# Optimization experiments

Measured on AMD Instinct MI355X. Metric: run time of the kernel, lower is better.

Reference implementation:

```python
import jax, jax.numpy as jnp
import numpy as np

N_NODES = 100000
N_EDGES = 600000
DIM = 128


def mish(v):
    return v * jnp.tanh(jax.nn.softplus(v))


def setup_inputs() -> dict:
    key = jax.random.key(0)
    ks = jax.random.split(key, 10)
    x = jax.random.normal(ks[0], (N_NODES, DIM), dtype=jnp.float32)
    edge_attr = jax.random.normal(ks[1], (N_EDGES, DIM), dtype=jnp.float32)
    # build edges with src < dst guaranteed (so the torch mask edge_index[0]<edge_index[1] is all True)
    a = jax.random.randint(ks[2], (N_EDGES,), 0, N_NODES - 1)
    b = jax.random.randint(ks[3], (N_EDGES,), 0, N_NODES - 1)
    src = jnp.minimum(a, b)
    dst = jnp.maximum(a, b) + (src == jnp.maximum(a, b)).astype(a.dtype)  # fix ties, stays < N_NODES
    edge_index = jnp.stack([src, dst]).astype(jnp.int64)
    s1 = 1.0 / np.sqrt(2 * DIM)
    s2 = 1.0 / np.sqrt(DIM)
    eW1 = jax.random.uniform(ks[4], (2 * DIM, DIM), jnp.float32, -s1, s1)
    eW2 = jax.random.uniform(ks[5], (DIM, DIM), jnp.float32, -s2, s2)
    nW1 = jax.random.uniform(ks[6], (2 * DIM, DIM), jnp.float32, -s1, s1)
    nW2 = jax.random.uniform(ks[7], (DIM, DIM), jnp.float32, -s2, s2)
    zb = jnp.zeros((DIM,), jnp.float32)
    return {"x": x, "edge_attr": edge_attr, "edge_index": edge_index,
            "eW1": eW1, "eb1": zb, "eW2": eW2, "eb2": zb,
            "nW1": nW1, "nb1": zb, "nW2": nW2, "nb2": zb}


def reference(x, edge_attr, edge_index, eW1, eb1, eW2, eb2, nW1, nb1, nW2, nb2):
    src, dst = edge_index[0], edge_index[1]
    # mask src < dst is all-True by construction of edge_index (see setup_inputs)
    e_in = jnp.concatenate([edge_attr, x[src] + x[dst]], axis=-1)      # [E, 2d]
    e = mish(e_in @ eW1 + eb1) @ eW2 + eb2                             # [E, d]
    agg = jax.ops.segment_sum(edge_attr, dst, num_segments=N_NODES)    # scatter_sum over dst, padded to N
    x_in = jnp.concatenate([x, agg], axis=-1)                          # [N, 2d]
    x_out = mish(x_in @ nW1 + nb1) @ nW2 + nb2                         # [N, d]
    return x_out, e
```

## Files before the change

kernel.cpp:

```cpp
#include <hip/hip_runtime.h>

#define N_NODES 100000
#define N_EDGES 600000
#define DIM 128

typedef __attribute__((ext_vector_type(8))) short short8;
typedef __attribute__((ext_vector_type(4))) float floatx4;
typedef unsigned short ushort_t;

#define MFMA(a,b,c) __builtin_amdgcn_mfma_f32_16x16x32_bf16((a),(b),(c),0,0,0)

__device__ __forceinline__ void bar_sync() {
    asm volatile("s_waitcnt lgkmcnt(0)" ::: "memory");
    __builtin_amdgcn_s_barrier();
    asm volatile("" ::: "memory");
}

__device__ __forceinline__ unsigned short f2bf(float f) {
    unsigned int u = __float_as_uint(f);
    u += 0x7fffu + ((u >> 16) & 1u);
    return (unsigned short)(u >> 16);
}

__device__ __forceinline__ short8 pack8(const float4& a, const float4& b) {
    short8 r;
    r[0] = (short)f2bf(a.x); r[1] = (short)f2bf(a.y);
    r[2] = (short)f2bf(a.z); r[3] = (short)f2bf(a.w);
    r[4] = (short)f2bf(b.x); r[5] = (short)f2bf(b.y);
    r[6] = (short)f2bf(b.z); r[7] = (short)f2bf(b.w);
    return r;
}

__device__ __forceinline__ short8 addpack_bf(short8 a, short8 b) {
    short8 r;
    #pragma unroll
    for (int i = 0; i < 8; ++i) {
        const float fa = __uint_as_float(((unsigned int)(unsigned short)a[i]) << 16);
        const float fb = __uint_as_float(((unsigned int)(unsigned short)b[i]) << 16);
        r[i] = (short)f2bf(fa + fb);
    }
    return r;
}

__device__ __forceinline__ float mish_f(float v) {
    if (v > 30.0f) return v;
    float t = __expf(v);
    float z = 1.0f + t;
    float z2 = z * z;
    return v * (z2 - 1.0f) / (z2 + 1.0f);
}

__device__ __forceinline__ short8 load_bfrag(const float* __restrict__ W,
                                             int ct, int kt, int lane) {
    const float* p = W + (size_t)(kt * 32 + (lane >> 4) * 8) * DIM + ct * 16 + (lane & 15);
    short8 r;
    #pragma unroll
    for (int j = 0; j < 8; ++j) r[j] = (short)f2bf(p[(size_t)j * DIM]);
    return r;
}

__device__ __forceinline__ void mlp_core(
    const ushort_t* __restrict__ s_in, ushort_t* __restrict__ s_h,
    const short8 (&w1f)[8], const short8 (&w2f)[4],
    float b1v, float b2v, float* __restrict__ out, int wave, int lane)
{
    const int r0 = lane & 15, q = lane >> 4, sw = lane & 7;

    floatx4 acc0 = {0.f,0.f,0.f,0.f}, acc1 = acc0;
    #pragma unroll
    for (int kt = 0; kt < 8; ++kt) {
        const int g = kt * 4 + q;
        short8 a0 = *(const short8*)&s_in[r0 * 256 + (g ^ sw) * 8];
        short8 a1 = *(const short8*)&s_in[(16 + r0) * 256 + (g ^ sw) * 8];
        acc0 = MFMA(a0, w1f[kt], acc0);
        acc1 = MFMA(a1, w1f[kt], acc1);
    }

    const int colg = wave * 2 + (r0 >> 3);
    const int bq   = r0 & 7;
    #pragma unroll
    for (int i = 0; i < 4; ++i) {
        int row = q * 4 + i;
        s_h[row * 128 + (colg ^ (row & 7)) * 8 + bq] = f2bf(mish_f(acc0[i] + b1v));
        row += 16;
        s_h[row * 128 + (colg ^ (row & 7)) * 8 + bq] = f2bf(mish_f(acc1[i] + b1v));
    }
    bar_sync();

    floatx4 c0 = {0.f,0.f,0.f,0.f}, c1 = c0;
    #pragma unroll
    for (int kt = 0; kt < 4; ++kt) {
        const int g = kt * 4 + q;
        short8 a0 = *(const short8*)&s_h[r0 * 128 + (g ^ sw) * 8];
        short8 a1 = *(const short8*)&s_h[(16 + r0) * 128 + (g ^ sw) * 8];
        c0 = MFMA(a0, w2f[kt], c0);
        c1 = MFMA(a1, w2f[kt], c1);
    }

    const int col = wave * 16 + r0;
    #pragma unroll
    for (int i = 0; i < 4; ++i) {
        __builtin_nontemporal_store(c0[i] + b2v, &out[(size_t)(q * 4 + i) * DIM + col]);
        __builtin_nontemporal_store(c1[i] + b2v, &out[(size_t)(16 + q * 4 + i) * DIM + col]);
    }
}


__global__ __launch_bounds__(256)
void zero_u4(uint4* __restrict__ p, int n4) {
    const int i = blockIdx.x * 256 + threadIdx.x;
    if (i < n4) p[i] = make_uint4(0u, 0u, 0u, 0u);
}

__global__ __launch_bounds__(256)
void xbf_kernel(const float* __restrict__ x, ushort_t* __restrict__ x_bf) {
    const int i = blockIdx.x * 256 + threadIdx.x;
    const float* p = x + (size_t)i * 8;
    *(short8*)&x_bf[(size_t)i * 8] = pack8(*(const float4*)p, *(const float4*)(p + 4));
}

__global__ __launch_bounds__(256)
void hist_kernel(const int* __restrict__ dst_idx, int* __restrict__ deg) {
    const int e = blockIdx.x * 256 + threadIdx.x;
    if (e < N_EDGES) atomicAdd(&deg[dst_idx[e]], 1);
}

__global__ __launch_bounds__(1024)
void scan_a(const int* __restrict__ deg, int* __restrict__ tmp, int* __restrict__ partials) {
    __shared__ int sm[1024];
    const int t = threadIdx.x;
    const int i = blockIdx.x * 1024 + t;
    const int v = (i < N_NODES) ? deg[i] : 0;
    sm[t] = v; __syncthreads();
    for (int d = 1; d < 1024; d <<= 1) {
        int u = (t >= d) ? sm[t - d] : 0; __syncthreads();
        sm[t] += u; __syncthreads();
    }
    if (i < N_NODES) tmp[i] = sm[t] - v;
    if (t == 1023) partials[blockIdx.x] = sm[t];
}

__global__ __launch_bounds__(128)
void scan_b(const int* __restrict__ partials, int* __restrict__ poffs) {
    __shared__ int sm[128];
    const int t = threadIdx.x;
    const int v = (t < 98) ? partials[t] : 0;
    sm[t] = v; __syncthreads();
    for (int d = 1; d < 128; d <<= 1) {
        int u = (t >= d) ? sm[t - d] : 0; __syncthreads();
        sm[t] += u; __syncthreads();
    }
    poffs[t] = sm[t] - v;
}

__global__ __launch_bounds__(1024)
void scan_c(const int* __restrict__ tmp, const int* __restrict__ poffs,
            int* __restrict__ rowptr, int* __restrict__ cursor) {
    const int t = threadIdx.x;
    const int i = blockIdx.x * 1024 + t;
    if (i < N_NODES) {
        const int v = tmp[i] + poffs[blockIdx.x];
        rowptr[i] = v; cursor[i] = v;
    }
    if (i == 0) rowptr[N_NODES] = N_EDGES;
}

__global__ __launch_bounds__(256)
void scatter_kernel(const int* __restrict__ dst_idx, int* __restrict__ cursor,
                    int* __restrict__ perm) {
    const int e = blockIdx.x * 256 + threadIdx.x;
    if (e < N_EDGES) {
        const int pos = atomicAdd(&cursor[dst_idx[e]], 1);
        perm[pos] = e;
    }
}


__global__ __launch_bounds__(256)
void agg_kernel(const float* __restrict__ edge_attr, const int* __restrict__ rowptr,
                const int* __restrict__ perm, ushort_t* __restrict__ agg_bf) {
    const int g  = (blockIdx.x << 4) + (threadIdx.x >> 4);
    const int ln = threadIdx.x & 15;
    const int k0 = rowptr[g], k1 = rowptr[g + 1];
    float4 A0 = {0.f,0.f,0.f,0.f}, A1 = A0, B0 = A0, B1 = A0;
    int e0 = 0, e1 = 0, e2 = 0, e3 = 0;
    if (k0 < k1)     e0 = perm[k0];
    if (k0 + 1 < k1) e1 = perm[k0 + 1];
    if (k0 + 2 < k1) e2 = perm[k0 + 2];
    if (k0 + 3 < k1) e3 = perm[k0 + 3];
    int k = k0;
    for (; k + 3 < k1; k += 4) {
        const float* p0 = edge_attr + (size_t)e0 * DIM + ln * 8;
        const float* p1 = edge_attr + (size_t)e1 * DIM + ln * 8;
        const float* p2 = edge_attr + (size_t)e2 * DIM + ln * 8;
        const float* p3 = edge_attr + (size_t)e3 * DIM + ln * 8;
        const float4 a0 = *(const float4*)p0, a1 = *(const float4*)(p0 + 4);
        const float4 b0 = *(const float4*)p1, b1 = *(const float4*)(p1 + 4);
        const float4 c0 = *(const float4*)p2, c1 = *(const float4*)(p2 + 4);
        const float4 d0 = *(const float4*)p3, d1 = *(const float4*)(p3 + 4);
        if (k + 4 < k1) e0 = perm[k + 4];
        if (k + 5 < k1) e1 = perm[k + 5];
        if (k + 6 < k1) e2 = perm[k + 6];
        if (k + 7 < k1) e3 = perm[k + 7];
        A0.x += a0.x + c0.x; A0.y += a0.y + c0.y; A0.z += a0.z + c0.z; A0.w += a0.w + c0.w;
        A1.x += a1.x + c1.x; A1.y += a1.y + c1.y; A1.z += a1.z + c1.z; A1.w += a1.w + c1.w;
        B0.x += b0.x + d0.x; B0.y += b0.y + d0.y; B0.z += b0.z + d0.z; B0.w += b0.w + d0.w;
        B1.x += b1.x + d1.x; B1.y += b1.y + d1.y; B1.z += b1.z + d1.z; B1.w += b1.w + d1.w;
    }
    const int rem = k1 - k;
    if (rem > 0) {
        const float* p = edge_attr + (size_t)e0 * DIM + ln * 8;
        const float4 v0 = *(const float4*)p, v1 = *(const float4*)(p + 4);
        A0.x += v0.x; A0.y += v0.y; A0.z += v0.z; A0.w += v0.w;
        A1.x += v1.x; A1.y += v1.y; A1.z += v1.z; A1.w += v1.w;
    }
    if (rem > 1) {
        const float* p = edge_attr + (size_t)e1 * DIM + ln * 8;
        const float4 v0 = *(const float4*)p, v1 = *(const float4*)(p + 4);
        B0.x += v0.x; B0.y += v0.y; B0.z += v0.z; B0.w += v0.w;
        B1.x += v1.x; B1.y += v1.y; B1.z += v1.z; B1.w += v1.w;
    }
    if (rem > 2) {
        const float* p = edge_attr + (size_t)e2 * DIM + ln * 8;
        const float4 v0 = *(const float4*)p, v1 = *(const float4*)(p + 4);
        A0.x += v0.x; A0.y += v0.y; A0.z += v0.z; A0.w += v0.w;
        A1.x += v1.x; A1.y += v1.y; A1.z += v1.z; A1.w += v1.w;
    }
    A0.x += B0.x; A0.y += B0.y; A0.z += B0.z; A0.w += B0.w;
    A1.x += B1.x; A1.y += B1.y; A1.z += B1.z; A1.w += B1.w;
    *(short8*)&agg_bf[(size_t)g * DIM + ln * 8] = pack8(A0, A1);
}


__global__ __launch_bounds__(512)
void edge_kernel(const ushort_t* __restrict__ x_bf, const float* __restrict__ edge_attr,
                 const int* __restrict__ src_idx, const int* __restrict__ dst_idx,
                 const float* __restrict__ W1, const float* __restrict__ b1,
                 const float* __restrict__ W2, const float* __restrict__ b2,
                 float* __restrict__ e_out)
{
    __shared__ ushort_t s_in[32 * 256];
    __shared__ ushort_t s_h[32 * 128];
    const int tid = threadIdx.x, wave = tid >> 6, lane = tid & 63;

    short8 w1f[8], w2f[4];
    const float b1v = b1[wave * 16 + (lane & 15)];
    const float b2v = b2[wave * 16 + (lane & 15)];
    #pragma unroll
    for (int kt = 0; kt < 8; ++kt) w1f[kt] = load_bfrag(W1, wave, kt, lane);
    #pragma unroll
    for (int kt = 0; kt < 4; ++kt) w2f[kt] = load_bfrag(W2, wave, kt, lane);

    const int r = tid >> 4, gq = tid & 15, swr = r & 7;
    ushort_t* w_ea = &s_in[r * 256 + (gq ^ swr) * 8];
    ushort_t* w_x  = &s_in[r * 256 + ((16 + gq) ^ swr) * 8];

    const int ntiles = N_EDGES / 32;
    int t = blockIdx.x;
    float4 ea0, ea1;
    short8 xsb, xdb;
    if (t < ntiles) {
        const int k = t * 32 + r;
        const int s = src_idx[k], d = dst_idx[k];
        const float* pe = edge_attr + (size_t)k * DIM + gq * 8;
        ea0 = *(const float4*)pe; ea1 = *(const float4*)(pe + 4);
        xsb = *(const short8*)&x_bf[(size_t)s * DIM + gq * 8];
        xdb = *(const short8*)&x_bf[(size_t)d * DIM + gq * 8];
    }
    for (; t < ntiles; t += gridDim.x) {
        *(short8*)w_ea = pack8(ea0, ea1);
        *(short8*)w_x  = addpack_bf(xsb, xdb);

        const int tn = t + gridDim.x;
        const bool more = tn < ntiles;
        int sN = 0, dN = 0;
        if (more) {
            const float* pe = edge_attr + (size_t)(tn * 32 + r) * DIM + gq * 8;
            ea0 = *(const float4*)pe; ea1 = *(const float4*)(pe + 4);
            const int k = tn * 32 + r;
            sN = src_idx[k]; dN = dst_idx[k];
        }
        bar_sync();
        if (more) {
            xsb = *(const short8*)&x_bf[(size_t)sN * DIM + gq * 8];
            xdb = *(const short8*)&x_bf[(size_t)dN * DIM + gq * 8];
        }
        mlp_core(s_in, s_h, w1f, w2f, b1v, b2v,
                 e_out + (size_t)t * 32 * DIM, wave, lane);
    }
}

__global__ __launch_bounds__(512)
void node_kernel(const float* __restrict__ x, const ushort_t* __restrict__ agg_bf,
                 const float* __restrict__ W1, const float* __restrict__ b1,
                 const float* __restrict__ W2, const float* __restrict__ b2,
                 float* __restrict__ x_out)
{
    __shared__ ushort_t s_in[32 * 256];
    __shared__ ushort_t s_h[32 * 128];
    const int tid = threadIdx.x, wave = tid >> 6, lane = tid & 63;

    short8 w1f[8], w2f[4];
    const float b1v = b1[wave * 16 + (lane & 15)];
    const float b2v = b2[wave * 16 + (lane & 15)];
    #pragma unroll
    for (int kt = 0; kt < 8; ++kt) w1f[kt] = load_bfrag(W1, wave, kt, lane);
    #pragma unroll
    for (int kt = 0; kt < 4; ++kt) w2f[kt] = load_bfrag(W2, wave, kt, lane);

    const int r = tid >> 4, gq = tid & 15, swr = r & 7;
    ushort_t* w_xp = &s_in[r * 256 + (gq ^ swr) * 8];
    ushort_t* w_ag = &s_in[r * 256 + ((16 + gq) ^ swr) * 8];

    const int ntiles = N_NODES / 32;
    int t = blockIdx.x;
    float4 xv0, xv1;
    short8 ag;
    if (t < ntiles) {
        const float* px = x + (size_t)(t * 32 + r) * DIM + gq * 8;
        xv0 = *(const float4*)px; xv1 = *(const float4*)(px + 4);
        ag  = *(const short8*)&agg_bf[(size_t)(t * 32 + r) * DIM + gq * 8];
    }
    for (; t < ntiles; t += gridDim.x) {
        *(short8*)w_xp = pack8(xv0, xv1);
        *(short8*)w_ag = ag;
        const int tn = t + gridDim.x;
        if (tn < ntiles) {
            const float* px = x + (size_t)(tn * 32 + r) * DIM + gq * 8;
            xv0 = *(const float4*)px; xv1 = *(const float4*)(px + 4);
            ag  = *(const short8*)&agg_bf[(size_t)(tn * 32 + r) * DIM + gq * 8];
        }
        bar_sync();
        mlp_core(s_in, s_h, w1f, w2f, b1v, b2v,
                 x_out + (size_t)t * 32 * DIM, wave, lane);
    }
}

extern "C" void kernel_launch(void* const* d_in, const int* in_sizes, int n_in,
                              void* d_out, int out_size, void* d_ws, size_t ws_size,
                              hipStream_t stream)
{
    const float* x         = (const float*)d_in[0];
    const float* edge_attr = (const float*)d_in[1];
    const int*   ei        = (const int*)d_in[2];
    const float* eW1 = (const float*)d_in[3];
    const float* eb1 = (const float*)d_in[4];
    const float* eW2 = (const float*)d_in[5];
    const float* eb2 = (const float*)d_in[6];
    const float* nW1 = (const float*)d_in[7];
    const float* nb1 = (const float*)d_in[8];
    const float* nW2 = (const float*)d_in[9];
    const float* nb2 = (const float*)d_in[10];

    float* out   = (float*)d_out;
    float* x_out = out;
    float* e_out = out + (size_t)N_NODES * DIM;

    const int* src_idx = ei;
    const int* dst_idx = ei + N_EDGES;

    int* wsi      = (int*)d_ws;
    int* deg      = wsi;
    int* tmp      = wsi + 100352;
    int* rowptr   = wsi + 200704;
    int* cursor   = wsi + 301056;
    int* perm     = wsi + 401408;
    int* partials = wsi + 1001408;
    int* poffs    = wsi + 1001536;
    ushort_t* agg_bf = (ushort_t*)(wsi + 1001664);

    ushort_t* x_bf = (ushort_t*)x_out;

    const int egrid = (N_EDGES + 255) / 256;
    zero_u4       <<<dim3(98),    dim3(256),  0, stream>>>((uint4*)deg, 25088);
    xbf_kernel    <<<dim3(6250),  dim3(256),  0, stream>>>(x, x_bf);
    hist_kernel   <<<dim3(egrid), dim3(256),  0, stream>>>(dst_idx, deg);
    scan_a        <<<dim3(98),    dim3(1024), 0, stream>>>(deg, tmp, partials);
    scan_b        <<<dim3(1),     dim3(128),  0, stream>>>(partials, poffs);
    scan_c        <<<dim3(98),    dim3(1024), 0, stream>>>(tmp, poffs, rowptr, cursor);
    scatter_kernel<<<dim3(egrid), dim3(256),  0, stream>>>(dst_idx, cursor, perm);

    agg_kernel<<<dim3(6250), dim3(256), 0, stream>>>(edge_attr, rowptr, perm, agg_bf);

    edge_kernel<<<dim3(2048), dim3(512), 0, stream>>>(
        x_bf, edge_attr, src_idx, dst_idx, eW1, eb1, eW2, eb2, e_out);

    node_kernel<<<dim3(2048), dim3(512), 0, stream>>>(
        x, agg_bf, nW1, nb1, nW2, nb2, x_out);
}
```

Measured before the change: 363.2 us.

## Co-launch aggregation with edge MLP in one kernel, merge zero and bf16 cast

Puts the memory-bound segment-sum aggregation and the MFMA-bound edge MLP into one launch, with block-index ranges choosing the role, so the two can overlap on the GPU. It also merges the degree-zeroing and the x-to-bf16 conversion into a single launch. The goal is fewer launches and better overlap of bandwidth-bound and compute-bound work. In exchange, agg blocks now carry the edge kernel's 512-thread launch and LDS footprint, which can lower occupancy, and finish times across the two roles may be unbalanced.

```diff
diff --git a/kernel.cpp b/kernel.cpp
--- a/kernel.cpp
+++ b/kernel.cpp
@@ -3,6 +3,9 @@
 #define N_NODES 100000
 #define N_EDGES 600000
 #define DIM 128
+
+#define AGG_BLOCKS  1024
+#define EDGE_BLOCKS 2048
 
 typedef __attribute__((ext_vector_type(8))) short short8;
 typedef __attribute__((ext_vector_type(4))) float floatx4;
@@ -107,14 +110,15 @@
 
 
 __global__ __launch_bounds__(256)
-void zero_u4(uint4* __restrict__ p, int n4) {
-    const int i = blockIdx.x * 256 + threadIdx.x;
-    if (i < n4) p[i] = make_uint4(0u, 0u, 0u, 0u);
-}
-
-__global__ __launch_bounds__(256)
-void xbf_kernel(const float* __restrict__ x, ushort_t* __restrict__ x_bf) {
-    const int i = blockIdx.x * 256 + threadIdx.x;
+void zero_xbf_kernel(uint4* __restrict__ deg4, int n4,
+                     const float* __restrict__ x, ushort_t* __restrict__ x_bf) {
+    const int b = blockIdx.x;
+    if (b < 98) {
+        const int i = b * 256 + threadIdx.x;
+        if (i < n4) deg4[i] = make_uint4(0u, 0u, 0u, 0u);
+        return;
+    }
+    const int i = (b - 98) * 256 + threadIdx.x;
     const float* p = x + (size_t)i * 8;
     *(short8*)&x_bf[(size_t)i * 8] = pack8(*(const float4*)p, *(const float4*)(p + 4));
 }
@@ -176,72 +180,77 @@
 }
 
 
-__global__ __launch_bounds__(256)
-void agg_kernel(const float* __restrict__ edge_attr, const int* __restrict__ rowptr,
-                const int* __restrict__ perm, ushort_t* __restrict__ agg_bf) {
-    const int g  = (blockIdx.x << 4) + (threadIdx.x >> 4);
-    const int ln = threadIdx.x & 15;
-    const int k0 = rowptr[g], k1 = rowptr[g + 1];
-    float4 A0 = {0.f,0.f,0.f,0.f}, A1 = A0, B0 = A0, B1 = A0;
-    int e0 = 0, e1 = 0, e2 = 0, e3 = 0;
-    if (k0 < k1)     e0 = perm[k0];
-    if (k0 + 1 < k1) e1 = perm[k0 + 1];
-    if (k0 + 2 < k1) e2 = perm[k0 + 2];
-    if (k0 + 3 < k1) e3 = perm[k0 + 3];
-    int k = k0;
-    for (; k + 3 < k1; k += 4) {
-        const float* p0 = edge_attr + (size_t)e0 * DIM + ln * 8;
-        const float* p1 = edge_attr + (size_t)e1 * DIM + ln * 8;
-        const float* p2 = edge_attr + (size_t)e2 * DIM + ln * 8;
-        const float* p3 = edge_attr + (size_t)e3 * DIM + ln * 8;
-        const float4 a0 = *(const float4*)p0, a1 = *(const float4*)(p0 + 4);
-        const float4 b0 = *(const float4*)p1, b1 = *(const float4*)(p1 + 4);
-        const float4 c0 = *(const float4*)p2, c1 = *(const float4*)(p2 + 4);
-        const float4 d0 = *(const float4*)p3, d1 = *(const float4*)(p3 + 4);
-        if (k + 4 < k1) e0 = perm[k + 4];
-        if (k + 5 < k1) e1 = perm[k + 5];
-        if (k + 6 < k1) e2 = perm[k + 6];
-        if (k + 7 < k1) e3 = perm[k + 7];
-        A0.x += a0.x + c0.x; A0.y += a0.y + c0.y; A0.z += a0.z + c0.z; A0.w += a0.w + c0.w;
-        A1.x += a1.x + c1.x; A1.y += a1.y + c1.y; A1.z += a1.z + c1.z; A1.w += a1.w + c1.w;
-        B0.x += b0.x + d0.x; B0.y += b0.y + d0.y; B0.z += b0.z + d0.z; B0.w += b0.w + d0.w;
-        B1.x += b1.x + d1.x; B1.y += b1.y + d1.y; B1.z += b1.z + d1.z; B1.w += b1.w + d1.w;
-    }
-    const int rem = k1 - k;
-    if (rem > 0) {
-        const float* p = edge_attr + (size_t)e0 * DIM + ln * 8;
-        const float4 v0 = *(const float4*)p, v1 = *(const float4*)(p + 4);
-        A0.x += v0.x; A0.y += v0.y; A0.z += v0.z; A0.w += v0.w;
-        A1.x += v1.x; A1.y += v1.y; A1.z += v1.z; A1.w += v1.w;
-    }
-    if (rem > 1) {
-        const float* p = edge_attr + (size_t)e1 * DIM + ln * 8;
-        const float4 v0 = *(const float4*)p, v1 = *(const float4*)(p + 4);
-        B0.x += v0.x; B0.y += v0.y; B0.z += v0.z; B0.w += v0.w;
-        B1.x += v1.x; B1.y += v1.y; B1.z += v1.z; B1.w += v1.w;
-    }
-    if (rem > 2) {
-        const float* p = edge_attr + (size_t)e2 * DIM + ln * 8;
-        const float4 v0 = *(const float4*)p, v1 = *(const float4*)(p + 4);
-        A0.x += v0.x; A0.y += v0.y; A0.z += v0.z; A0.w += v0.w;
-        A1.x += v1.x; A1.y += v1.y; A1.z += v1.z; A1.w += v1.w;
-    }
-    A0.x += B0.x; A0.y += B0.y; A0.z += B0.z; A0.w += B0.w;
-    A1.x += B1.x; A1.y += B1.y; A1.z += B1.z; A1.w += B1.w;
-    *(short8*)&agg_bf[(size_t)g * DIM + ln * 8] = pack8(A0, A1);
-}
-
-
 __global__ __launch_bounds__(512)
-void edge_kernel(const ushort_t* __restrict__ x_bf, const float* __restrict__ edge_attr,
-                 const int* __restrict__ src_idx, const int* __restrict__ dst_idx,
-                 const float* __restrict__ W1, const float* __restrict__ b1,
-                 const float* __restrict__ W2, const float* __restrict__ b2,
-                 float* __restrict__ e_out)
+void edge_agg_kernel(const ushort_t* __restrict__ x_bf,
+                     const float* __restrict__ edge_attr,
+                     const int* __restrict__ src_idx, const int* __restrict__ dst_idx,
+                     const int* __restrict__ rowptr, const int* __restrict__ perm,
+                     const float* __restrict__ W1, const float* __restrict__ b1,
+                     const float* __restrict__ W2, const float* __restrict__ b2,
+                     float* __restrict__ e_out, ushort_t* __restrict__ agg_bf)
 {
     __shared__ ushort_t s_in[32 * 256];
     __shared__ ushort_t s_h[32 * 128];
-    const int tid = threadIdx.x, wave = tid >> 6, lane = tid & 63;
+    const int tid = threadIdx.x;
+
+    if (blockIdx.x < AGG_BLOCKS) {
+        const int sub = tid >> 4;
+        const int ln  = tid & 15;
+        for (int grp = blockIdx.x; grp < N_NODES / 32; grp += AGG_BLOCKS) {
+            const int g = grp * 32 + sub;
+            const int k0 = rowptr[g], k1 = rowptr[g + 1];
+            float4 A0 = {0.f,0.f,0.f,0.f}, A1 = A0, B0 = A0, B1 = A0;
+            int e0 = 0, e1 = 0, e2 = 0, e3 = 0;
+            if (k0 < k1)     e0 = perm[k0];
+            if (k0 + 1 < k1) e1 = perm[k0 + 1];
+            if (k0 + 2 < k1) e2 = perm[k0 + 2];
+            if (k0 + 3 < k1) e3 = perm[k0 + 3];
+            int k = k0;
+            for (; k + 3 < k1; k += 4) {
+                const float* p0 = edge_attr + (size_t)e0 * DIM + ln * 8;
+                const float* p1 = edge_attr + (size_t)e1 * DIM + ln * 8;
+                const float* p2 = edge_attr + (size_t)e2 * DIM + ln * 8;
+                const float* p3 = edge_attr + (size_t)e3 * DIM + ln * 8;
+                const float4 a0 = *(const float4*)p0, a1 = *(const float4*)(p0 + 4);
+                const float4 b0 = *(const float4*)p1, b1 = *(const float4*)(p1 + 4);
+                const float4 c0 = *(const float4*)p2, c1 = *(const float4*)(p2 + 4);
+                const float4 d0 = *(const float4*)p3, d1 = *(const float4*)(p3 + 4);
+                if (k + 4 < k1) e0 = perm[k + 4];
+                if (k + 5 < k1) e1 = perm[k + 5];
+                if (k + 6 < k1) e2 = perm[k + 6];
+                if (k + 7 < k1) e3 = perm[k + 7];
+                A0.x += a0.x + c0.x; A0.y += a0.y + c0.y; A0.z += a0.z + c0.z; A0.w += a0.w + c0.w;
+                A1.x += a1.x + c1.x; A1.y += a1.y + c1.y; A1.z += a1.z + c1.z; A1.w += a1.w + c1.w;
+                B0.x += b0.x + d0.x; B0.y += b0.y + d0.y; B0.z += b0.z + d0.z; B0.w += b0.w + d0.w;
+                B1.x += b1.x + d1.x; B1.y += b1.y + d1.y; B1.z += b1.z + d1.z; B1.w += b1.w + d1.w;
+            }
+            const int rem = k1 - k;
+            if (rem > 0) {
+                const float* p = edge_attr + (size_t)e0 * DIM + ln * 8;
+                const float4 v0 = *(const float4*)p, v1 = *(const float4*)(p + 4);
+                A0.x += v0.x; A0.y += v0.y; A0.z += v0.z; A0.w += v0.w;
+                A1.x += v1.x; A1.y += v1.y; A1.z += v1.z; A1.w += v1.w;
+            }
+            if (rem > 1) {
+                const float* p = edge_attr + (size_t)e1 * DIM + ln * 8;
+                const float4 v0 = *(const float4*)p, v1 = *(const float4*)(p + 4);
+                B0.x += v0.x; B0.y += v0.y; B0.z += v0.z; B0.w += v0.w;
+                B1.x += v1.x; B1.y += v1.y; B1.z += v1.z; B1.w += v1.w;
+            }
+            if (rem > 2) {
+                const float* p = edge_attr + (size_t)e2 * DIM + ln * 8;
+                const float4 v0 = *(const float4*)p, v1 = *(const float4*)(p + 4);
+                A0.x += v0.x; A0.y += v0.y; A0.z += v0.z; A0.w += v0.w;
+                A1.x += v1.x; A1.y += v1.y; A1.z += v1.z; A1.w += v1.w;
+            }
+            A0.x += B0.x; A0.y += B0.y; A0.z += B0.z; A0.w += B0.w;
+            A1.x += B1.x; A1.y += B1.y; A1.z += B1.z; A1.w += B1.w;
+            *(short8*)&agg_bf[(size_t)g * DIM + ln * 8] = pack8(A0, A1);
+        }
+        return;
+    }
+
+    const int wave = tid >> 6, lane = tid & 63;
 
     short8 w1f[8], w2f[4];
     const float b1v = b1[wave * 16 + (lane & 15)];
@@ -256,7 +265,7 @@
     ushort_t* w_x  = &s_in[r * 256 + ((16 + gq) ^ swr) * 8];
 
     const int ntiles = N_EDGES / 32;
-    int t = blockIdx.x;
+    int t = blockIdx.x - AGG_BLOCKS;
     float4 ea0, ea1;
     short8 xsb, xdb;
     if (t < ntiles) {
@@ -267,11 +276,11 @@
         xsb = *(const short8*)&x_bf[(size_t)s * DIM + gq * 8];
         xdb = *(const short8*)&x_bf[(size_t)d * DIM + gq * 8];
     }
-    for (; t < ntiles; t += gridDim.x) {
+    for (; t < ntiles; t += EDGE_BLOCKS) {
         *(short8*)w_ea = pack8(ea0, ea1);
         *(short8*)w_x  = addpack_bf(xsb, xdb);
 
-        const int tn = t + gridDim.x;
+        const int tn = t + EDGE_BLOCKS;
         const bool more = tn < ntiles;
         int sN = 0, dN = 0;
         if (more) {
@@ -372,18 +381,17 @@
     ushort_t* x_bf = (ushort_t*)x_out;
 
     const int egrid = (N_EDGES + 255) / 256;
-    zero_u4       <<<dim3(98),    dim3(256),  0, stream>>>((uint4*)deg, 25088);
-    xbf_kernel    <<<dim3(6250),  dim3(256),  0, stream>>>(x, x_bf);
+    zero_xbf_kernel<<<dim3(98 + 6250), dim3(256), 0, stream>>>(
+        (uint4*)deg, 25088, x, x_bf);
     hist_kernel   <<<dim3(egrid), dim3(256),  0, stream>>>(dst_idx, deg);
     scan_a        <<<dim3(98),    dim3(1024), 0, stream>>>(deg, tmp, partials);
     scan_b        <<<dim3(1),     dim3(128),  0, stream>>>(partials, poffs);
     scan_c        <<<dim3(98),    dim3(1024), 0, stream>>>(tmp, poffs, rowptr, cursor);
     scatter_kernel<<<dim3(egrid), dim3(256),  0, stream>>>(dst_idx, cursor, perm);
 
-    agg_kernel<<<dim3(6250), dim3(256), 0, stream>>>(edge_attr, rowptr, perm, agg_bf);
-
-    edge_kernel<<<dim3(2048), dim3(512), 0, stream>>>(
-        x_bf, edge_attr, src_idx, dst_idx, eW1, eb1, eW2, eb2, e_out);
+    edge_agg_kernel<<<dim3(AGG_BLOCKS + EDGE_BLOCKS), dim3(512), 0, stream>>>(
+        x_bf, edge_attr, src_idx, dst_idx, rowptr, perm,
+        eW1, eb1, eW2, eb2, e_out, agg_bf);
 
     node_kernel<<<dim3(2048), dim3(512), 0, stream>>>(
         x, agg_bf, nW1, nb1, nW2, nb2, x_out);
```

New measurement: 367.2 us. Within noise of the previous version (+1.1%).
